# Optimization experiments

Measured on AMD Instinct MI355X. Metric: run time of the kernel, lower is better.

Reference implementation:

```python
import jax, jax.numpy as jnp
import numpy as np

IN_C, HID, OUT_C, N = 128, 128, 1, 8192


def setup_inputs() -> dict:
    key = jax.random.key(0)
    ks = jax.random.split(key, 16)
    s_in = 1.0 / np.sqrt(IN_C)
    s_h = 1.0 / np.sqrt(HID)
    inp = {
        "x": jax.random.normal(ks[0], (N, IN_C), dtype=jnp.float32),
        "Wq": jax.random.uniform(ks[1], (IN_C, HID), minval=-s_in, maxval=s_in),
        "bq": jnp.zeros((HID,), jnp.float32),
        "Wk": jax.random.uniform(ks[2], (IN_C, HID), minval=-s_in, maxval=s_in),
        "bk": jnp.zeros((HID,), jnp.float32),
        "Wv": jax.random.uniform(ks[3], (IN_C, HID), minval=-s_in, maxval=s_in),
        "bv": jnp.zeros((HID,), jnp.float32),
        "Wskip": jax.random.uniform(ks[4], (IN_C, HID), minval=-s_in, maxval=s_in),
        "bskip": jnp.zeros((HID,), jnp.float32),
        "W1": jax.random.uniform(ks[5], (HID, HID), minval=-s_h, maxval=s_h),
        "b1": jnp.zeros((HID,), jnp.float32),
        "W2": jax.random.uniform(ks[6], (HID, OUT_C), minval=-s_h, maxval=s_h),
        "b2": jnp.zeros((OUT_C,), jnp.float32),
        "k": 7,
    }
    return inp


def _transformer_conv(x, Wq, bq, Wk, bk, Wv, bv, Wskip, bskip):
    # PyG TransformerConv, heads=1, concat=False, root_weight=True, over a
    # complete graph (no self-loops) -> dense attention with masked diagonal.
    q = x @ Wq + bq  # [N, H]
    kk = x @ Wk + bk
    v = x @ Wv + bv
    d = q.shape[-1]
    scores = (q @ kk.T) / jnp.sqrt(jnp.asarray(d, q.dtype))  # [N, N]
    n = x.shape[0]
    eye = jnp.eye(n, dtype=bool)
    scores = jnp.where(eye, -jnp.inf, scores)
    attn = jax.nn.softmax(scores, axis=-1)
    out = attn @ v
    return out + x @ Wskip + bskip


def _knn_indices(h, k):
    # k nearest neighbors (excluding self) in squared-euclidean distance.
    sq = jnp.sum(h * h, axis=1)
    d2 = sq[:, None] + sq[None, :] - 2.0 * (h @ h.T)  # [N, N]
    n = h.shape[0]
    d2 = jnp.where(jnp.eye(n, dtype=bool), jnp.inf, d2)
    _, idx = jax.lax.top_k(-d2, k)  # [N, k] neighbor (source) indices
    return idx


def _gcn_conv(h, idx, W, b, k):
    # Each node has exactly k incoming edges + self-loop => gcn_norm weight
    # is uniformly 1/(k+1) on every edge.
    m = h @ W  # [N, d]
    agg = (m[idx].sum(axis=1) + m) / jnp.asarray(k + 1, h.dtype)
    return agg + b


def reference(x, Wq, bq, Wk, bk, Wv, bv, Wskip, bskip, W1, b1, W2, b2, k):
    h = _transformer_conv(x, Wq, bq, Wk, bk, Wv, bv, Wskip, bskip)  # [N, HID]
    idx = _knn_indices(h, k)  # KNNGraph(k) on embeddings
    h1 = jax.nn.relu(_gcn_conv(h, idx, W1, b1, k))
    out = _gcn_conv(h1, idx, W2, b2, k)  # [N, OUT_C]
    return out
```

## Files before the change

kernel.cpp:

```cpp
#include <hip/hip_runtime.h>
#include <cmath>


typedef unsigned short ushort_t;

constexpr int   NN    = 8192;
constexpr int   DD    = 128;
constexpr int   KNB   = 7;
constexpr int   NL    = 10;
constexpr int   NCAND = 12;
constexpr float SCALE = 0.088388347648318447f;

using bf16x8 = __attribute__((ext_vector_type(8))) short;
using f32x4  = __attribute__((ext_vector_type(4))) float;

#define MFMA16(a, b, c) __builtin_amdgcn_mfma_f32_16x16x32_bf16((a), (b), (c), 0, 0, 0)

__device__ __forceinline__ ushort_t f2b(float f) {
    union { float f; unsigned int u; } v; v.f = f;
    return (ushort_t)((v.u + 0x8000u) >> 16);
}
__device__ __forceinline__ float b2f(ushort_t h) {
    union { unsigned int u; float f; } v; v.u = ((unsigned int)h) << 16;
    return v.f;
}

__device__ __forceinline__ void gload16(const void* g, void* l) {
    __builtin_amdgcn_global_load_lds(
        (const __attribute__((address_space(1))) unsigned int*)g,
        (__attribute__((address_space(3))) unsigned int*)l, 16, 0, 0);
}

__device__ __forceinline__ unsigned umin_(unsigned a, unsigned b) { return a < b ? a : b; }
__device__ __forceinline__ unsigned umax_(unsigned a, unsigned b) { return a > b ? a : b; }

template<int K>
__device__ __forceinline__ void ins_asc(unsigned* a, unsigned x)
{
    #pragma unroll
    for (int p = K - 1; p >= 1; --p)
        a[p] = umin_(umax_(x, a[p - 1]), a[p]);
    a[0] = umin_(a[0], x);
}

constexpr int PR = 8;
__global__ __launch_bounds__(128)
void proj_kernel(const float* __restrict__ x,
                 const float* __restrict__ Wq, const float* __restrict__ bq,
                 const float* __restrict__ Wk, const float* __restrict__ bk,
                 const float* __restrict__ Wv, const float* __restrict__ bv,
                 const float* __restrict__ Ws, const float* __restrict__ bs,
                 ushort_t* __restrict__ Qhi, ushort_t* __restrict__ Qlo,
                 ushort_t* __restrict__ Khi, ushort_t* __restrict__ Klo,
                 ushort_t* __restrict__ VThi, ushort_t* __restrict__ VTlo,
                 float* __restrict__ HS)
{
    __shared__ float xs[PR][DD];
    const int i0 = blockIdx.x * PR, t = threadIdx.x;
    #pragma unroll
    for (int r = 0; r < PR; ++r) xs[r][t] = x[(i0 + r) * DD + t];
    __syncthreads();
    float aq[PR], ak[PR], av[PR], ah[PR];
    #pragma unroll
    for (int r = 0; r < PR; ++r) { aq[r] = 0.f; ak[r] = 0.f; av[r] = 0.f; ah[r] = 0.f; }
    #pragma unroll 4
    for (int c = 0; c < DD; ++c) {
        const float wq = Wq[c * DD + t], wk = Wk[c * DD + t];
        const float wv = Wv[c * DD + t], ws = Ws[c * DD + t];
        #pragma unroll
        for (int r = 0; r < PR; ++r) {
            const float xv = xs[r][c];
            aq[r] = fmaf(xv, wq, aq[r]); ak[r] = fmaf(xv, wk, ak[r]);
            av[r] = fmaf(xv, wv, av[r]); ah[r] = fmaf(xv, ws, ah[r]);
        }
    }
    ushort_t vh8[PR], vl8[PR];
    #pragma unroll
    for (int r = 0; r < PR; ++r) {
        const int o = (i0 + r) * DD + t;
        const float q = aq[r] + bq[t];
        const float k = ak[r] + bk[t];
        const ushort_t qh = f2b(q); Qhi[o] = qh; Qlo[o] = f2b(q - b2f(qh));
        const ushort_t kh = f2b(k); Khi[o] = kh; Klo[o] = f2b(k - b2f(kh));
        const float v = av[r] + bv[t];
        const ushort_t vh = f2b(v);
        vh8[r] = vh; vl8[r] = f2b(v - b2f(vh));
        HS[o] = ah[r] + bs[t];
    }
    *reinterpret_cast<uint4*>(VThi + (size_t)t * NN + i0) =
        *reinterpret_cast<const uint4*>(vh8);
    *reinterpret_cast<uint4*>(VTlo + (size_t)t * NN + i0) =
        *reinterpret_cast<const uint4*>(vl8);
}

constexpr int ANS  = 8;
constexpr int AKS  = NN / ANS;
constexpr int BK   = 32;
constexpr int PSTR = 40;
constexpr int KSTR = 136;

__global__ __launch_bounds__(256, 2)
void attn_kernel(const ushort_t* __restrict__ Qhi, const ushort_t* __restrict__ Qlo,
                 const ushort_t* __restrict__ Khg, const ushort_t* __restrict__ Klg,
                 const ushort_t* __restrict__ Vhg, const ushort_t* __restrict__ Vlg,
                 float* __restrict__ Opart, float* __restrict__ lpart)
{
    __shared__ __align__(16) ushort_t Khs[2][BK * DD];
    __shared__ __align__(16) ushort_t Kls[2][BK * DD];
    __shared__ __align__(16) ushort_t Vhs[2][DD * BK];
    __shared__ __align__(16) ushort_t Vls[2][DD * BK];
    __shared__ __align__(16) ushort_t Phs[4][16 * PSTR];
    __shared__ __align__(16) ushort_t Pls[4][16 * PSTR];

    const int t  = threadIdx.x;
    const int w  = t >> 6, l = t & 63;
    const int lc = l & 15, lq = l >> 4;
    const int b  = blockIdx.x;
    const int s  = b >> 6;
    const int qb = b & 63;
    const int i0 = qb * 128;
    const int k0 = s * AKS;
    ushort_t* Pwh = Phs[w];
    ushort_t* Pwl = Pls[w];

    const int lrK = w * 4 + (l >> 4);
    const int kchunk = ((l & 15) ^ (lrK & 7)) * 8;
    const ushort_t* gKh = Khg + (size_t)(k0 + lrK) * DD + kchunk;
    const ushort_t* gKl = Klg + (size_t)(k0 + lrK) * DD + kchunk;
    const int lrV = w * 16 + (l >> 2);
    const int vchunk = ((l & 3) ^ ((l >> 3) & 3)) * 8;
    const ushort_t* gVh = Vhg + (size_t)lrV * NN + k0 + vchunk;
    const ushort_t* gVl = Vlg + (size_t)lrV * NN + k0 + vchunk;

#define STAGE_K(buf, koff) do {                                              \
    gload16(gKh + (size_t)(koff) * DD,        &Khs[buf][(w * 4) * DD]);      \
    gload16(gKh + (size_t)((koff) + 16) * DD, &Khs[buf][(16 + w * 4) * DD]); \
    gload16(gKl + (size_t)(koff) * DD,        &Kls[buf][(w * 4) * DD]);      \
    gload16(gKl + (size_t)((koff) + 16) * DD, &Kls[buf][(16 + w * 4) * DD]); \
  } while (0)
#define STAGE_V(buf, koff) do {                                              \
    gload16(gVh + (koff),                     &Vhs[buf][(w * 16) * BK]);     \
    gload16(gVh + (size_t)64 * NN + (koff),   &Vhs[buf][(64 + w * 16) * BK]);\
    gload16(gVl + (koff),                     &Vls[buf][(w * 16) * BK]);     \
    gload16(gVl + (size_t)64 * NN + (koff),   &Vls[buf][(64 + w * 16) * BK]);\
  } while (0)
#define LGKM0() asm volatile("s_waitcnt lgkmcnt(0)" ::: "memory")
#define VMW(n)  asm volatile("s_waitcnt vmcnt(" #n ")" ::: "memory")
#define BARRIER() do { __builtin_amdgcn_s_barrier(); \
                       __builtin_amdgcn_sched_barrier(0); } while (0)

    bf16x8 qh[2][4], ql[2][4];
    #pragma unroll
    for (int sub = 0; sub < 2; ++sub) {
        const int row = i0 + w * 32 + sub * 16 + lc;
        #pragma unroll
        for (int kb = 0; kb < 4; ++kb) {
            qh[sub][kb] = *reinterpret_cast<const bf16x8*>(Qhi + row * DD + kb * 32 + lq * 8);
            ql[sub][kb] = *reinterpret_cast<const bf16x8*>(Qlo + row * DD + kb * 32 + lq * 8);
        }
    }

    const f32x4 zz = {0.f, 0.f, 0.f, 0.f};
    f32x4 oacc[2][8];
    #pragma unroll
    for (int sub = 0; sub < 2; ++sub)
        #pragma unroll
        for (int ft = 0; ft < 8; ++ft) oacc[sub][ft] = zz;
    float lrow[2] = {0.f, 0.f};

    bf16x8 pah[2] = {}, pal[2] = {};
    const int vc = (lq ^ ((lc >> 1) & 3)) * 8;

    STAGE_K(0, 0);
    STAGE_K(1, BK);
    STAGE_V(0, 0);
    VMW(8);
    BARRIER();

    constexpr int NT = AKS / BK;
    for (int it = 0; it < NT; ++it) {
        const int jt  = k0 + it * BK;
        const int cur = it & 1;
        const ushort_t* Kh = Khs[cur];
        const ushort_t* Kl = Kls[cur];
        const ushort_t* Vph = Vhs[cur ^ 1];
        const ushort_t* Vpl = Vls[cur ^ 1];

        f32x4 sacc[2][2];
        #pragma unroll
        for (int sub = 0; sub < 2; ++sub)
            #pragma unroll
            for (int kt = 0; kt < 2; ++kt) sacc[sub][kt] = zz;
        __builtin_amdgcn_s_setprio(1);
        #pragma unroll
        for (int kt = 0; kt < 2; ++kt) {
            const int kro = (kt * 16 + lc) * DD;
            #pragma unroll
            for (int kb = 0; kb < 4; ++kb) {
                const int cp = ((kb * 4 + lq) ^ (lc & 7)) * 8;
                const bf16x8 kh = *reinterpret_cast<const bf16x8*>(&Kh[kro + cp]);
                const bf16x8 kl = *reinterpret_cast<const bf16x8*>(&Kl[kro + cp]);
                #pragma unroll
                for (int sub = 0; sub < 2; ++sub) {
                    sacc[sub][kt] = MFMA16(kh, qh[sub][kb], sacc[sub][kt]);
                    sacc[sub][kt] = MFMA16(kh, ql[sub][kb], sacc[sub][kt]);
                    sacc[sub][kt] = MFMA16(kl, qh[sub][kb], sacc[sub][kt]);
                }
            }
        }
        __builtin_amdgcn_s_setprio(0);

        if (it > 0) {
            __builtin_amdgcn_s_setprio(1);
            #pragma unroll
            for (int ft = 0; ft < 8; ++ft) {
                const bf16x8 vh = *reinterpret_cast<const bf16x8*>(
                    &Vph[(ft * 16 + lc) * BK + vc]);
                const bf16x8 vl = *reinterpret_cast<const bf16x8*>(
                    &Vpl[(ft * 16 + lc) * BK + vc]);
                #pragma unroll
                for (int sub = 0; sub < 2; ++sub) {
                    oacc[sub][ft] = MFMA16(pah[sub], vh, oacc[sub][ft]);
                    oacc[sub][ft] = MFMA16(pal[sub], vh, oacc[sub][ft]);
                    oacc[sub][ft] = MFMA16(pah[sub], vl, oacc[sub][ft]);
                }
            }
            __builtin_amdgcn_s_setprio(0);
        }

        LGKM0();
        BARRIER();

        if (it <= NT - 3) STAGE_K(cur, (it + 2) * BK);
        if (it <= NT - 2) STAGE_V(cur ^ 1, (it + 1) * BK);

        if ((jt & ~127) == i0) {
            #pragma unroll
            for (int sub = 0; sub < 2; ++sub) {
                const int gq = i0 + w * 32 + sub * 16 + lc;
                #pragma unroll
                for (int kt = 0; kt < 2; ++kt)
                    #pragma unroll
                    for (int r = 0; r < 4; ++r) {
                        const int gk = jt + kt * 16 + lq * 4 + r;
                        if (gk == gq) sacc[sub][kt][r] = -INFINITY;
                    }
            }
        }
        #pragma unroll
        for (int sub = 0; sub < 2; ++sub) {
            #pragma unroll
            for (int kt = 0; kt < 2; ++kt) {
                unsigned wh[2], wl[2];
                #pragma unroll
                for (int rr = 0; rr < 2; ++rr) {
                    const float p0 = __expf(sacc[sub][kt][rr * 2 + 0] * SCALE);
                    const float p1 = __expf(sacc[sub][kt][rr * 2 + 1] * SCALE);
                    lrow[sub] += p0;
                    lrow[sub] += p1;
                    unsigned hpk;
                    asm("v_cvt_pk_bf16_f32 %0, %1, %2"
                        : "=v"(hpk) : "v"(p0), "v"(p1));
                    wh[rr] = hpk;
                    const float h0 = __uint_as_float(hpk << 16);
                    const float h1 = __uint_as_float(hpk & 0xFFFF0000u);
                    unsigned lpk;
                    asm("v_cvt_pk_bf16_f32 %0, %1, %2"
                        : "=v"(lpk) : "v"(p0 - h0), "v"(p1 - h1));
                    wl[rr] = lpk;
                }
                const int eo = lc * PSTR + kt * 16 + lq * 4;
                *reinterpret_cast<uint2*>(&Pwh[eo]) = make_uint2(wh[0], wh[1]);
                *reinterpret_cast<uint2*>(&Pwl[eo]) = make_uint2(wl[0], wl[1]);
            }
            pah[sub] = *reinterpret_cast<const bf16x8*>(&Pwh[lc * PSTR + lq * 8]);
            pal[sub] = *reinterpret_cast<const bf16x8*>(&Pwl[lc * PSTR + lq * 8]);
        }

        if (it <= NT - 3)      { VMW(8); }
        else if (it == NT - 2) { VMW(4); }
        else                   { VMW(0); }
        BARRIER();
    }
    {
        const ushort_t* Vh = Vhs[(NT - 1) & 1];
        const ushort_t* Vl = Vls[(NT - 1) & 1];
        #pragma unroll
        for (int ft = 0; ft < 8; ++ft) {
            const bf16x8 vh = *reinterpret_cast<const bf16x8*>(
                &Vh[(ft * 16 + lc) * BK + vc]);
            const bf16x8 vl = *reinterpret_cast<const bf16x8*>(
                &Vl[(ft * 16 + lc) * BK + vc]);
            #pragma unroll
            for (int sub = 0; sub < 2; ++sub) {
                oacc[sub][ft] = MFMA16(pah[sub], vh, oacc[sub][ft]);
                oacc[sub][ft] = MFMA16(pal[sub], vh, oacc[sub][ft]);
                oacc[sub][ft] = MFMA16(pah[sub], vl, oacc[sub][ft]);
            }
        }
    }
#undef STAGE_K
#undef STAGE_V
#undef LGKM0
#undef VMW
#undef BARRIER

    #pragma unroll
    for (int sub = 0; sub < 2; ++sub) {
        float ps = lrow[sub];
        ps += __shfl_xor(ps, 16, 64);
        ps += __shfl_xor(ps, 32, 64);
        lrow[sub] = ps;
    }
    #pragma unroll
    for (int sub = 0; sub < 2; ++sub) {
        #pragma unroll
        for (int r = 0; r < 4; ++r) {
            const int row = i0 + w * 32 + sub * 16 + lq * 4 + r;
            float* po = Opart + ((size_t)s * NN + row) * DD;
            #pragma unroll
            for (int ft = 0; ft < 8; ++ft) po[ft * 16 + lc] = oacc[sub][ft][r];
        }
        if (l < 16)
            lpart[s * NN + i0 + w * 32 + sub * 16 + l] = lrow[sub];
    }
}

__global__ __launch_bounds__(256)
void attn_merge_kernel(const float* __restrict__ Opart, const float* __restrict__ lpart,
                       const float* __restrict__ HS, float* __restrict__ H,
                       ushort_t* __restrict__ Hhi, float* __restrict__ SQ,
                       const float* __restrict__ W1, float* __restrict__ M1)
{
    __shared__ float xs[8][132];
    const int t = threadIdx.x;
    const int gid = blockIdx.x * 256 + t;
    const int i = gid >> 5;
    const int f = (gid & 31) * 4;
    float ls = 0.f;
    float4 o = {0.f, 0.f, 0.f, 0.f};
    #pragma unroll
    for (int s = 0; s < ANS; ++s) {
        ls += lpart[s * NN + i];
        const float4 ov = *reinterpret_cast<const float4*>(
            Opart + ((size_t)s * NN + i) * DD + f);
        o.x += ov.x; o.y += ov.y; o.z += ov.z; o.w += ov.w;
    }
    const float4 hs = *reinterpret_cast<const float4*>(HS + i * DD + f);
    const float inv = 1.f / ls;
    float4 h;
    h.x = o.x * inv + hs.x; h.y = o.y * inv + hs.y;
    h.z = o.z * inv + hs.z; h.w = o.w * inv + hs.w;
    *reinterpret_cast<float4*>(H + i * DD + f) = h;
    *reinterpret_cast<float4*>(&xs[t >> 5][f]) = h;
    ushort_t hb[4] = {f2b(h.x), f2b(h.y), f2b(h.z), f2b(h.w)};
    *reinterpret_cast<uint2*>(Hhi + i * DD + f) = *reinterpret_cast<const uint2*>(hb);
    float sq = h.x * h.x + h.y * h.y + h.z * h.z + h.w * h.w;
    sq += __shfl_xor(sq, 1, 64);
    sq += __shfl_xor(sq, 2, 64);
    sq += __shfl_xor(sq, 4, 64);
    sq += __shfl_xor(sq, 8, 64);
    sq += __shfl_xor(sq, 16, 64);
    if ((t & 31) == 0) SQ[i] = sq;

    __syncthreads();
    const int col = t & 127, half = t >> 7;
    float a[4] = {0.f, 0.f, 0.f, 0.f};
    #pragma unroll 4
    for (int c = 0; c < DD; ++c) {
        const float wv = W1[c * DD + col];
        #pragma unroll
        for (int r = 0; r < 4; ++r)
            a[r] = fmaf(xs[half * 4 + r][c], wv, a[r]);
    }
    const int n0 = blockIdx.x * 8 + half * 4;
    #pragma unroll
    for (int r = 0; r < 4; ++r)
        M1[(n0 + r) * DD + col] = a[r];
}

constexpr int KNSL = 16;
constexpr int KSL  = NN / KNSL;

__global__ __launch_bounds__(256, 4)
void knn_kernel(const ushort_t* __restrict__ Hhi, const float* __restrict__ SQg,
                unsigned* __restrict__ candV)
{
    __shared__ __align__(16) ushort_t Khi[64 * KSTR];
    __shared__ __align__(16) float sqs[64];

    const int t  = threadIdx.x;
    const int w  = t >> 6, l = t & 63;
    const int lc = l & 15, lq = l >> 4;
    const int b  = blockIdx.x;
    const int s  = b >> 6;
    const int qb = b & 63;
    const int i0 = qb * 128;
    const int k0 = s * KSL;

    const int kr = t >> 4, kc2 = t & 15;

    const int gq0 = i0 + w * 32 + lc;
    const int gq1 = gq0 + 16;
    const float sqi0 = SQg[gq0];
    const float sqi1 = SQg[gq1];

    bf16x8 qf[2][4];
    #pragma unroll
    for (int sub = 0; sub < 2; ++sub) {
        const int row = i0 + w * 32 + sub * 16 + lc;
        #pragma unroll
        for (int kb = 0; kb < 4; ++kb)
            qf[sub][kb] = *reinterpret_cast<const bf16x8*>(Hhi + row * DD + kb * 32 + lq * 8);
    }

    unsigned lists[2][NL];
    #pragma unroll
    for (int sub = 0; sub < 2; ++sub)
        #pragma unroll
        for (int p = 0; p < NL; ++p) lists[sub][p] = 0xFFFFFFFFu;

    uint4 pk[4]; float psq;
    #pragma unroll
    for (int p = 0; p < 4; ++p)
        pk[p] = *reinterpret_cast<const uint4*>(Hhi + (k0 + kr + p * 16) * DD + kc2 * 8);
    psq = (t < 64) ? SQg[k0 + t] : 0.f;

    const f32x4 zz = {0.f, 0.f, 0.f, 0.f};
    for (int jt0 = 0; jt0 < KSL; jt0 += 64) {
        const int jt = k0 + jt0;
        __syncthreads();
        #pragma unroll
        for (int p = 0; p < 4; ++p)
            *reinterpret_cast<uint4*>(&Khi[(kr + p * 16) * KSTR + kc2 * 8]) = pk[p];
        if (t < 64) sqs[t] = psq;
        __syncthreads();
        if (jt0 + 64 < KSL) {
            const int jn = jt + 64;
            #pragma unroll
            for (int p = 0; p < 4; ++p)
                pk[p] = *reinterpret_cast<const uint4*>(Hhi + (jn + kr + p * 16) * DD + kc2 * 8);
            psq = (t < 64) ? SQg[jn + t] : 0.f;
        }

        f32x4 acc[2][4];
        #pragma unroll
        for (int sub = 0; sub < 2; ++sub)
            #pragma unroll
            for (int kt = 0; kt < 4; ++kt) acc[sub][kt] = zz;
        #pragma unroll
        for (int kt = 0; kt < 4; ++kt) {
            #pragma unroll
            for (int kb = 0; kb < 4; ++kb) {
                const bf16x8 kf = *reinterpret_cast<const bf16x8*>(
                    &Khi[(kt * 16 + lc) * KSTR + kb * 32 + lq * 8]);
                acc[0][kt] = MFMA16(kf, qf[0][kb], acc[0][kt]);
                acc[1][kt] = MFMA16(kf, qf[1][kb], acc[1][kt]);
            }
        }

        const bool ovl = ((jt & ~127) == i0);
        #pragma unroll
        for (int kt = 0; kt < 4; ++kt) {
            const float4 sq4 = *reinterpret_cast<const float4*>(&sqs[kt * 16 + lq * 4]);
            const float sqj[4] = {sq4.x, sq4.y, sq4.z, sq4.w};
            #pragma unroll
            for (int r = 0; r < 4; ++r) {
                const int gk = jt + kt * 16 + lq * 4 + r;
                float d0 = fmaf(-2.f, acc[0][kt][r], sqi0 + sqj[r]);
                float d1 = fmaf(-2.f, acc[1][kt][r], sqi1 + sqj[r]);
                if (ovl) {
                    if (gk == gq0) d0 = INFINITY;
                    if (gk == gq1) d1 = INFINITY;
                }
                const unsigned u0 = (__float_as_uint(d0) & 0xFFFFE000u) | (unsigned)gk;
                const unsigned u1 = (__float_as_uint(d1) & 0xFFFFE000u) | (unsigned)gk;
                ins_asc<NL>(lists[0], u0);
                ins_asc<NL>(lists[1], u1);
            }
        }
    }

    __syncthreads();
    unsigned* msw = reinterpret_cast<unsigned*>(Khi) + w * (16 * 4 * NL);
    #pragma unroll
    for (int sub = 0; sub < 2; ++sub) {
        #pragma unroll
        for (int p = 0; p < NL; ++p)
            msw[lc * (4 * NL) + lq * NL + p] = lists[sub][p];
        __syncthreads();
        if (lq == 0) {
            unsigned bk[NL];
            #pragma unroll
            for (int p = 0; p < NL; ++p) bk[p] = msw[lc * (4 * NL) + p];
            #pragma unroll
            for (int o = 1; o < 4; ++o)
                #pragma unroll
                for (int e = 0; e < NL; ++e)
                    ins_asc<NL>(bk, msw[lc * (4 * NL) + o * NL + e]);
            const int node = i0 + w * 32 + sub * 16 + lc;
            #pragma unroll
            for (int p = 0; p < NL; ++p)
                candV[((size_t)s * NL + p) * NN + node] = bk[p];
        }
        __syncthreads();
    }
}

__global__ __launch_bounds__(64)
void knn_merge_kernel(const unsigned* __restrict__ candV, int* __restrict__ CAND)
{
    const int q = blockIdx.x * 64 + threadIdx.x;
    unsigned bk[NCAND];
    #pragma unroll
    for (int p = 0; p < NCAND; ++p) bk[p] = 0xFFFFFFFFu;
    for (int s = 0; s < KNSL; ++s)
        #pragma unroll
        for (int e = 0; e < NL; ++e)
            ins_asc<NCAND>(bk, candV[((size_t)s * NL + e) * NN + q]);
    #pragma unroll
    for (int p = 0; p < NCAND; ++p)
        CAND[q * NCAND + p] = (int)(bk[p] & 8191u);
}

__global__ __launch_bounds__(256)
void rerank_kernel(const float* __restrict__ H, const float* __restrict__ SQ,
                   const int* __restrict__ CAND, int* __restrict__ IDX)
{
    const int t = threadIdx.x;
    const int w = t >> 6, l = t & 63;
    const int node = blockIdx.x * 4 + w;
    const float h0 = H[node * DD + l];
    const float h1 = H[node * DD + 64 + l];
    float dk[NCAND]; int di[NCAND];
    #pragma unroll
    for (int c = 0; c < NCAND; ++c) {
        const int j = CAND[node * NCAND + c];
        float p = h0 * H[j * DD + l] + h1 * H[j * DD + 64 + l];
        p += __shfl_xor(p, 1, 64);
        p += __shfl_xor(p, 2, 64);
        p += __shfl_xor(p, 4, 64);
        p += __shfl_xor(p, 8, 64);
        p += __shfl_xor(p, 16, 64);
        p += __shfl_xor(p, 32, 64);
        dk[c] = SQ[j] - 2.f * p;
        di[c] = j;
    }
    if (l == 0) {
        #pragma unroll
        for (int s = 0; s < KNB; ++s) {
            int best = s;
            #pragma unroll
            for (int c = s + 1; c < NCAND; ++c) {
                const bool lt = (dk[c] < dk[best]) ||
                                (dk[c] == dk[best] && di[c] < di[best]);
                if (lt) best = c;
            }
            const float tk = dk[s]; dk[s] = dk[best]; dk[best] = tk;
            const int   ti = di[s]; di[s] = di[best]; di[best] = ti;
            IDX[node * KNB + s] = di[s];
        }
    }
}

__global__ __launch_bounds__(256)
void g1m2_kernel(const float* __restrict__ M1, const int* __restrict__ IDX,
                 const float* __restrict__ b1, const float* __restrict__ W2,
                 float* __restrict__ M2)
{
    const int t = threadIdx.x;
    const int w = t >> 6, l = t & 63;
    const int i = blockIdx.x * 4 + w;
    float s0 = M1[i * DD + l];
    float s1 = M1[i * DD + 64 + l];
    #pragma unroll
    for (int p = 0; p < KNB; ++p) {
        const int j = IDX[i * KNB + p];
        s0 += M1[j * DD + l];
        s1 += M1[j * DD + 64 + l];
    }
    const float g0 = fmaxf(s0 * 0.125f + b1[l], 0.f);
    const float g1 = fmaxf(s1 * 0.125f + b1[64 + l], 0.f);
    float r = g0 * W2[l] + g1 * W2[64 + l];
    r += __shfl_xor(r, 32, 64);
    r += __shfl_xor(r, 16, 64);
    r += __shfl_xor(r, 8, 64);
    r += __shfl_xor(r, 4, 64);
    r += __shfl_xor(r, 2, 64);
    r += __shfl_xor(r, 1, 64);
    if (l == 0) M2[i] = r;
}

__global__ __launch_bounds__(256)
void out_kernel(const float* __restrict__ M2, const int* __restrict__ IDX,
                const float* __restrict__ b2, float* __restrict__ out)
{
    const int i = blockIdx.x * 256 + threadIdx.x;
    if (i < NN) {
        float s = M2[i];
        #pragma unroll
        for (int p = 0; p < KNB; ++p) s += M2[IDX[i * KNB + p]];
        out[i] = s * 0.125f + b2[0];
    }
}

extern "C" void kernel_launch(void* const* d_in, const int* in_sizes, int n_in,
                              void* d_out, int out_size, void* d_ws, size_t ws_size,
                              hipStream_t stream)
{
    const float* x   = (const float*)d_in[0];
    const float* Wq  = (const float*)d_in[1];
    const float* bq  = (const float*)d_in[2];
    const float* Wk  = (const float*)d_in[3];
    const float* bk  = (const float*)d_in[4];
    const float* Wv  = (const float*)d_in[5];
    const float* bv  = (const float*)d_in[6];
    const float* Wsk = (const float*)d_in[7];
    const float* bsk = (const float*)d_in[8];
    const float* W1  = (const float*)d_in[9];
    const float* b1  = (const float*)d_in[10];
    const float* W2  = (const float*)d_in[11];
    const float* b2  = (const float*)d_in[12];

    constexpr size_t MB = 1024 * 1024;
    char* W = (char*)d_ws;
    ushort_t* Qhi  = (ushort_t*)(W + 0 * MB);
    ushort_t* Qlo  = (ushort_t*)(W + 2 * MB);
    ushort_t* Khi  = (ushort_t*)(W + 4 * MB);
    ushort_t* Klo  = (ushort_t*)(W + 6 * MB);
    ushort_t* VThi = (ushort_t*)(W + 8 * MB);
    ushort_t* VTlo = (ushort_t*)(W + 10 * MB);
    float*    HS   = (float*)(W + 12 * MB);
    float*    H    = HS;
    ushort_t* Hhi  = Qhi;
    float* lpart = (float*)(W + 16 * MB);
    float* SQ    = (float*)(W + 16 * MB + 256 * 1024);
    float* M2    = SQ + NN;
    int*   IDX   = (int*)(M2 + NN);
    float*    Opart = (float*)(W + 17 * MB);
    unsigned* candV = (unsigned*)(W + 17 * MB);
    int*      CAND  = (int*)(W + 23 * MB);
    float*    M1    = (float*)(W + 49 * MB);

    proj_kernel<<<NN / PR, 128, 0, stream>>>(x, Wq, bq, Wk, bk, Wv, bv, Wsk, bsk,
                                             Qhi, Qlo, Khi, Klo, VThi, VTlo, HS);
    attn_kernel<<<ANS * 64, 256, 0, stream>>>(Qhi, Qlo, Khi, Klo, VThi, VTlo,
                                              Opart, lpart);
    attn_merge_kernel<<<(NN * 32) / 256, 256, 0, stream>>>(Opart, lpart, HS, H,
                                                           Hhi, SQ, W1, M1);
    knn_kernel<<<KNSL * 64, 256, 0, stream>>>(Hhi, SQ, candV);
    knn_merge_kernel<<<NN / 64, 64, 0, stream>>>(candV, CAND);
    rerank_kernel<<<NN / 4, 256, 0, stream>>>(H, SQ, CAND, IDX);
    g1m2_kernel<<<NN / 4, 256, 0, stream>>>(M1, IDX, b1, W2, M2);
    out_kernel<<<NN / 256, 256, 0, stream>>>(M2, IDX, b2, (float*)d_out);
}
```

Measured before the change: 320.0 us.

## Double-buffer KNN key tiles with async global-to-LDS loads and XOR swizzle

The KNN kernel previously staged key tiles through registers into a padded LDS tile, with two syncthreads per iteration. It now issues direct global-to-LDS loads into a double buffer, prefetching the next tile while the current tile's distance and insertion-sort work runs. An XOR chunk swizzle replaces the padding to avoid bank conflicts, and the squared-norm buffer is also double-buffered. The wait and barrier macros move to file scope so they can be shared. The cost is more LDS use (two unpadded tiles), which may affect occupancy.

```diff
diff --git a/kernel.cpp b/kernel.cpp
--- a/kernel.cpp
+++ b/kernel.cpp
@@ -15,6 +15,11 @@
 using f32x4  = __attribute__((ext_vector_type(4))) float;
 
 #define MFMA16(a, b, c) __builtin_amdgcn_mfma_f32_16x16x32_bf16((a), (b), (c), 0, 0, 0)
+
+#define LGKM0() asm volatile("s_waitcnt lgkmcnt(0)" ::: "memory")
+#define VMW(n)  asm volatile("s_waitcnt vmcnt(" #n ")" ::: "memory")
+#define BARRIER() do { __builtin_amdgcn_s_barrier(); \
+                       __builtin_amdgcn_sched_barrier(0); } while (0)
 
 __device__ __forceinline__ ushort_t f2b(float f) {
     union { float f; unsigned int u; } v; v.f = f;
@@ -97,7 +102,6 @@
 constexpr int AKS  = NN / ANS;
 constexpr int BK   = 32;
 constexpr int PSTR = 40;
-constexpr int KSTR = 136;
 
 __global__ __launch_bounds__(256, 2)
 void attn_kernel(const ushort_t* __restrict__ Qhi, const ushort_t* __restrict__ Qlo,
@@ -144,10 +148,6 @@
     gload16(gVl + (koff),                     &Vls[buf][(w * 16) * BK]);     \
     gload16(gVl + (size_t)64 * NN + (koff),   &Vls[buf][(64 + w * 16) * BK]);\
   } while (0)
-#define LGKM0() asm volatile("s_waitcnt lgkmcnt(0)" ::: "memory")
-#define VMW(n)  asm volatile("s_waitcnt vmcnt(" #n ")" ::: "memory")
-#define BARRIER() do { __builtin_amdgcn_s_barrier(); \
-                       __builtin_amdgcn_sched_barrier(0); } while (0)
 
     bf16x8 qh[2][4], ql[2][4];
     #pragma unroll
@@ -301,9 +301,6 @@
     }
 #undef STAGE_K
 #undef STAGE_V
-#undef LGKM0
-#undef VMW
-#undef BARRIER
 
     #pragma unroll
     for (int sub = 0; sub < 2; ++sub) {
@@ -386,8 +383,8 @@
 void knn_kernel(const ushort_t* __restrict__ Hhi, const float* __restrict__ SQg,
                 unsigned* __restrict__ candV)
 {
-    __shared__ __align__(16) ushort_t Khi[64 * KSTR];
-    __shared__ __align__(16) float sqs[64];
+    __shared__ __align__(16) ushort_t Khs[2][64 * DD];
+    __shared__ __align__(16) float sqs[2][64];
 
     const int t  = threadIdx.x;
     const int w  = t >> 6, l = t & 63;
@@ -398,7 +395,16 @@
     const int i0 = qb * 128;
     const int k0 = s * KSL;
 
-    const int kr = t >> 4, kc2 = t & 15;
+    const int srow = w * 4 + (l >> 4);
+    const int schunk = ((l & 15) ^ (srow & 7)) * 8;
+    const ushort_t* gH = Hhi + (size_t)(k0 + srow) * DD + schunk;
+
+#define KSTAGE(buf, koff) do {                                               \
+    gload16(gH + (size_t)((koff) +  0) * DD, &Khs[buf][( 0 + w * 4) * DD]);  \
+    gload16(gH + (size_t)((koff) + 16) * DD, &Khs[buf][(16 + w * 4) * DD]);  \
+    gload16(gH + (size_t)((koff) + 32) * DD, &Khs[buf][(32 + w * 4) * DD]);  \
+    gload16(gH + (size_t)((koff) + 48) * DD, &Khs[buf][(48 + w * 4) * DD]);  \
+  } while (0)
 
     const int gq0 = i0 + w * 32 + lc;
     const int gq1 = gq0 + 16;
@@ -420,28 +426,19 @@
         #pragma unroll
         for (int p = 0; p < NL; ++p) lists[sub][p] = 0xFFFFFFFFu;
 
-    uint4 pk[4]; float psq;
-    #pragma unroll
-    for (int p = 0; p < 4; ++p)
-        pk[p] = *reinterpret_cast<const uint4*>(Hhi + (k0 + kr + p * 16) * DD + kc2 * 8);
-    psq = (t < 64) ? SQg[k0 + t] : 0.f;
+    KSTAGE(0, 0);
+    float psq = (t < 64) ? SQg[k0 + t] : 0.f;
+    VMW(0);
+    BARRIER();
 
     const f32x4 zz = {0.f, 0.f, 0.f, 0.f};
-    for (int jt0 = 0; jt0 < KSL; jt0 += 64) {
-        const int jt = k0 + jt0;
-        __syncthreads();
-        #pragma unroll
-        for (int p = 0; p < 4; ++p)
-            *reinterpret_cast<uint4*>(&Khi[(kr + p * 16) * KSTR + kc2 * 8]) = pk[p];
-        if (t < 64) sqs[t] = psq;
-        __syncthreads();
-        if (jt0 + 64 < KSL) {
-            const int jn = jt + 64;
-            #pragma unroll
-            for (int p = 0; p < 4; ++p)
-                pk[p] = *reinterpret_cast<const uint4*>(Hhi + (jn + kr + p * 16) * DD + kc2 * 8);
-            psq = (t < 64) ? SQg[jn + t] : 0.f;
-        }
+    constexpr int KNT = KSL / 64;
+    for (int ti = 0; ti < KNT; ++ti) {
+        const int jt  = k0 + ti * 64;
+        const int cur = ti & 1;
+
+        if (t < 64) sqs[cur][t] = psq;
+        if (ti + 1 < KNT) psq = (t < 64) ? SQg[jt + 64 + t] : 0.f;
 
         f32x4 acc[2][4];
         #pragma unroll
@@ -450,19 +447,25 @@
             for (int kt = 0; kt < 4; ++kt) acc[sub][kt] = zz;
         #pragma unroll
         for (int kt = 0; kt < 4; ++kt) {
+            const int kro = (kt * 16 + lc) * DD;
             #pragma unroll
             for (int kb = 0; kb < 4; ++kb) {
-                const bf16x8 kf = *reinterpret_cast<const bf16x8*>(
-                    &Khi[(kt * 16 + lc) * KSTR + kb * 32 + lq * 8]);
+                const int cp = ((kb * 4 + lq) ^ (lc & 7)) * 8;
+                const bf16x8 kf = *reinterpret_cast<const bf16x8*>(&Khs[cur][kro + cp]);
                 acc[0][kt] = MFMA16(kf, qf[0][kb], acc[0][kt]);
                 acc[1][kt] = MFMA16(kf, qf[1][kb], acc[1][kt]);
             }
         }
 
+        LGKM0();
+        BARRIER();
+
+        if (ti + 1 < KNT) KSTAGE(cur ^ 1, (ti + 1) * 64);
+
         const bool ovl = ((jt & ~127) == i0);
         #pragma unroll
         for (int kt = 0; kt < 4; ++kt) {
-            const float4 sq4 = *reinterpret_cast<const float4*>(&sqs[kt * 16 + lq * 4]);
+            const float4 sq4 = *reinterpret_cast<const float4*>(&sqs[cur][kt * 16 + lq * 4]);
             const float sqj[4] = {sq4.x, sq4.y, sq4.z, sq4.w};
             #pragma unroll
             for (int r = 0; r < 4; ++r) {
@@ -479,10 +482,14 @@
                 ins_asc<NL>(lists[1], u1);
             }
         }
-    }
+
+        VMW(0);
+        BARRIER();
+    }
+#undef KSTAGE
 
     __syncthreads();
-    unsigned* msw = reinterpret_cast<unsigned*>(Khi) + w * (16 * 4 * NL);
+    unsigned* msw = reinterpret_cast<unsigned*>(Khs[0]) + w * (16 * 4 * NL);
     #pragma unroll
     for (int sub = 0; sub < 2; ++sub) {
         #pragma unroll
```

Result: faster. 309.1 us (-3.4%).
